# Kernel tuning notes

Measured on AMD Instinct MI355X. Metric: run time of the kernel, lower is better.

Reference implementation:

```python
import jax, jax.numpy as jnp
import numpy as np

B, N, D, H = 16, 4096, 768, 16
E = D // H  # head dim = 48
EPS = 1e-12  # F.normalize eps


def setup_inputs() -> dict:
    key = jax.random.key(0)
    ks = jax.random.split(key, 10)
    s = 0.02
    return {
        "x": jax.random.normal(ks[0], (B, N, D), dtype=jnp.float32),
        "wq": jax.random.normal(ks[1], (D, D), dtype=jnp.float32) * s,
        "bq": jnp.zeros((D,), dtype=jnp.float32),
        "wk": jax.random.normal(ks[2], (D, D), dtype=jnp.float32) * s,
        "bk": jnp.zeros((D,), dtype=jnp.float32),
        "wv": jax.random.normal(ks[3], (D, D), dtype=jnp.float32) * s,
        "bv": jnp.zeros((D,), dtype=jnp.float32),
        "wo": jax.random.normal(ks[4], (D, D), dtype=jnp.float32) * s,
        "bo": jnp.zeros((D,), dtype=jnp.float32),
        "tau": jnp.float32(H),  # scalar learnable temperature, init = num_heads
    }


def _l2norm_seq(t):
    # F.normalize(t, p=2, dim=1): normalize over sequence axis n of [b, n, h, e]
    nrm = jnp.sqrt(jnp.sum(t * t, axis=1, keepdims=True))
    return t / jnp.maximum(nrm, EPS)


def reference(x, wq, bq, wk, bk, wv, bv, wo, bo, tau):
    b, n, d = x.shape
    q = (x @ wq.T + bq).reshape(b, n, H, E)
    k = (x @ wk.T + bk).reshape(b, n, H, E)
    v = (x @ wv.T + bv).reshape(b, n, H, E)
    q = _l2norm_seq(q)
    k = _l2norm_seq(k)
    # cross-covariance attention over feature dim: [b, e, h, q]
    energy = jnp.einsum('bnhe,bnhq->behq', q, k)
    attn = jax.nn.softmax(energy, axis=-1)
    out = jnp.einsum('behq,bnhe->bnhq', attn / tau, v)  # [b, n, h, e]
    out = out.reshape(b, n, d)
    return out @ wo.T + bo
```

## Files before the change

kernel.cpp:

```cpp
#include <hip/hip_runtime.h>
#include <hip/hip_bf16.h>

typedef __attribute__((ext_vector_type(8))) short bf16x8_t;
typedef __attribute__((ext_vector_type(4))) float f32x4_t;
typedef __attribute__((ext_vector_type(4))) float fv4;
typedef __attribute__((ext_vector_type(4))) unsigned short us4_t;
typedef __attribute__((ext_vector_type(8))) unsigned short us8_t;

static constexpr int BB = 16, NN = 4096, DD = 768, HH = 16, EE = 48;

__device__ __forceinline__ unsigned short f2bf(float f) {
  unsigned int u = __float_as_uint(f);
  u += 0x7fffu + ((u >> 16) & 1u);
  return (unsigned short)(u >> 16);
}
__device__ __forceinline__ float bf2f(unsigned short s) {
  unsigned int u = ((unsigned int)s) << 16;
  return __uint_as_float(u);
}

__device__ __forceinline__ void load_lds16(const void* g, void* l) {
  __builtin_amdgcn_global_load_lds((const __attribute__((address_space(1))) void*)g,
                                   (__attribute__((address_space(3))) void*)l, 16, 0, 0);
}

template<int WRITE_THRU>
__device__ __forceinline__ void tcast64(const float* __restrict__ src, int sld,
                                        unsigned short* __restrict__ dst, int dld,
                                        unsigned short* __restrict__ thru, int tld, int t)
{
  __shared__ float L[64][65];
#pragma unroll
  for (int q = 0; q < 4; ++q) {
    const int fi = t + q * 256;
    const int r = fi >> 4, c4 = fi & 15;
    fv4 v = *(const fv4*)(src + (long)r * sld + c4 * 4);
    L[r][c4 * 4 + 0] = v.x; L[r][c4 * 4 + 1] = v.y;
    L[r][c4 * 4 + 2] = v.z; L[r][c4 * 4 + 3] = v.w;
    if (WRITE_THRU) {
      us4_t o; o.x = f2bf(v.x); o.y = f2bf(v.y); o.z = f2bf(v.z); o.w = f2bf(v.w);
      *(us4_t*)(thru + (long)r * tld + c4 * 4) = o;
    }
  }
  __syncthreads();
#pragma unroll
  for (int q = 0; q < 2; ++q) {
    const int wi = t + q * 256;
    const int rr = wi >> 3, ng = wi & 7;
    us8_t o;
#pragma unroll
    for (int j = 0; j < 8; ++j) o[j] = f2bf(L[ng * 8 + j][rr]);
    *(us8_t*)(dst + (long)rr * dld + ng * 8) = o;
  }
  __syncthreads();
}

__global__ __launch_bounds__(256) void transpose_cast_x(
    const float* __restrict__ x, unsigned short* __restrict__ xb,
    unsigned short* __restrict__ xbT)
{
  const int nx = blockIdx.x, dx = blockIdx.y, b = blockIdx.z;
  const int n0 = nx * 64, d0 = dx * 64;
  const float* src = x + ((long)b * NN + n0) * DD + d0;
  unsigned short* thru = xb + ((long)b * NN + n0) * DD + d0;
  unsigned short* dst = xbT + ((long)b * DD + d0) * NN + n0;
  tcast64<1>(src, DD, dst, NN, thru, DD, threadIdx.x);
}

__global__ __launch_bounds__(256) void small_cast(
    const float* __restrict__ wq, const float* __restrict__ wk, const float* __restrict__ wv,
    unsigned short* __restrict__ W2, unsigned short* __restrict__ wvT,
    float* __restrict__ zeros)
{
  const int blk = blockIdx.x, t = threadIdx.x;
  if (blk < 576) {
#pragma unroll
    for (int q = 0; q < 2; ++q) {
      long g = (long)blk * 512 + t * 2 + q;
      long e0 = g * 4;
      int row = (int)(e0 / DD), col = (int)(e0 % DD);
      const float* src = (row < DD) ? (wq + (long)row * DD + col)
                                    : (wk + (long)(row - DD) * DD + col);
      fv4 v = *(const fv4*)src;
      us4_t o; o.x = f2bf(v.x); o.y = f2bf(v.y); o.z = f2bf(v.z); o.w = f2bf(v.w);
      *(us4_t*)(W2 + e0) = o;
    }
  } else if (blk < 720) {
    const int tile = blk - 576;
    const int ti = tile / 12, tj = tile % 12;
    const int k0 = ti * 64, i0 = tj * 64;
    tcast64<0>(wv + (long)i0 * DD + k0, DD, wvT + (long)k0 * DD + i0, DD, nullptr, 0, t);
  } else {
#pragma unroll
    for (int q = 0; q < 4; ++q) zeros[t * 4 + q] = 0.f;
  }
}

__global__ __launch_bounds__(256) void colsum(
    const unsigned short* __restrict__ xbT, float* __restrict__ xsum)
{
  const int bx = blockIdx.x, b = blockIdx.y;
  const int wave = threadIdx.x >> 6, lane = threadIdx.x & 63;
  const int d = bx * 4 + wave;
  const unsigned short* row = xbT + ((long)b * DD + d) * NN;
  float s = 0.f;
#pragma unroll
  for (int it = 0; it < 8; ++it) {
    us8_t v = *(const us8_t*)(row + (it * 64 + lane) * 8);
#pragma unroll
    for (int j = 0; j < 8; ++j) s += bf2f(v[j]);
  }
#pragma unroll
  for (int off = 32; off > 0; off >>= 1) s += __shfl_down(s, off);
  if (lane == 0) xsum[(long)b * DD + d] = s;
}

template<int OUT_BF16>
__global__ __launch_bounds__(256) void gemm_bt(
    const unsigned short* __restrict__ A, int lda, long aStride,
    const unsigned short* __restrict__ Bt, int ldb, long bStride,
    void* __restrict__ Cv, int ldc, long cStride,
    const float* __restrict__ bias, long biasStride, int K)
{
  __shared__ unsigned short As[128 * 32];
  __shared__ unsigned short Bs[128 * 32];
  const int zb = blockIdx.z;
  const unsigned short* Ab = A + (long)zb * aStride;
  const unsigned short* Bb = Bt + (long)zb * bStride;
  const float* bz = bias + (long)zb * biasStride;
  const long m0 = (long)blockIdx.x * 128;
  const int n0 = blockIdx.y * 128;
  const int t = threadIdx.x;
  const int wave = t >> 6, lane = t & 63;
  const int wr = wave >> 1, wc = wave & 1;

  f32x4_t acc[4][4] = {};

  const int o0 = t * 16;
  const int row0 = o0 >> 6, kc0 = (o0 & 63) >> 1;
  const int o1 = 4096 + t * 16;
  const int row1 = o1 >> 6, kc1 = (o1 & 63) >> 1;
  unsigned short* ldsA = As + wave * 512;
  unsigned short* ldsB = Bs + wave * 512;

  for (int kt = 0; kt < K; kt += 32) {
    load_lds16(Ab + (m0 + row0) * (long)lda + kt + kc0, ldsA);
    load_lds16(Ab + (m0 + row1) * (long)lda + kt + kc1, ldsA + 2048);
    load_lds16(Bb + (long)(n0 + row0) * ldb + kt + kc0, ldsB);
    load_lds16(Bb + (long)(n0 + row1) * ldb + kt + kc1, ldsB + 2048);
    __syncthreads();
    bf16x8_t af[4], bfr[4];
    const int kofs = (lane >> 4) << 3;
#pragma unroll
    for (int f = 0; f < 4; ++f) {
      af[f]  = *(const bf16x8_t*)&As[(wr * 64 + f * 16 + (lane & 15)) * 32 + kofs];
      bfr[f] = *(const bf16x8_t*)&Bs[(wc * 64 + f * 16 + (lane & 15)) * 32 + kofs];
    }
#pragma unroll
    for (int i = 0; i < 4; ++i)
#pragma unroll
      for (int j = 0; j < 4; ++j)
        acc[i][j] = __builtin_amdgcn_mfma_f32_16x16x32_bf16(af[i], bfr[j], acc[i][j], 0, 0, 0);
    __syncthreads();
  }

  const int col_l = lane & 15;
  const int rbase = (lane >> 4) << 2;
#pragma unroll
  for (int i = 0; i < 4; ++i) {
#pragma unroll
    for (int r = 0; r < 4; ++r) {
      const long grow = m0 + wr * 64 + i * 16 + rbase + r;
      if (OUT_BF16) {
        unsigned short* crow = (unsigned short*)Cv + (long)zb * cStride + grow * ldc + n0 + wc * 64;
#pragma unroll
        for (int j = 0; j < 4; ++j) {
          int col = j * 16 + col_l;
          crow[col] = f2bf(acc[i][j][r] + bz[n0 + wc * 64 + col]);
        }
      } else {
        float* crow = (float*)Cv + (long)zb * cStride + grow * ldc + n0 + wc * 64;
#pragma unroll
        for (int j = 0; j < 4; ++j) {
          int col = j * 16 + col_l;
          crow[col] = acc[i][j][r] + bz[n0 + wc * 64 + col];
        }
      }
    }
  }
}

#define GP_STRIDE 2464

__global__ __launch_bounds__(256) void energy_partial2(
    const unsigned short* __restrict__ T, const unsigned short* __restrict__ W2,
    float* __restrict__ Gp)
{
  __shared__ unsigned short Ts[2][48 * 128];
  __shared__ unsigned short Ws[2][48 * 128];
  __shared__ float G_sh[2448];

  const int kc = blockIdx.x, h = blockIdx.y, b = blockIdx.z;
  const int t = threadIdx.x;
  const int wave = t >> 6, lane = t & 63;

  for (int i = t; i < 2448; i += 256) G_sh[i] = 0.f;

  f32x4_t accG[3][3] = {};
  f32x4_t accQ[3] = {};
  f32x4_t accK[3] = {};

  long qoff[3];
#pragma unroll
  for (int p = 0; p < 3; ++p) {
    const int L = p * 4096 + wave * 1024 + lane * 16;
    const int e = L >> 8;
    const int blk = (L >> 4) & 15;
    const int sblk = blk ^ (e & 7);
    qoff[p] = (long)e * DD + sblk * 8;
  }
  const unsigned short* Tq = T + ((long)b * 1536 + h * 48) * DD;
  const unsigned short* Tk = Tq + (long)DD * DD;
  const unsigned short* Wq = W2 + (long)h * 48 * DD;
  const unsigned short* Wk = Wq + (long)DD * DD;

  int foff[3];
#pragma unroll
  for (int f = 0; f < 3; ++f) {
    const int e = f * 16 + (lane & 15);
    foff[f] = e * 256 + (((wave * 4 + (lane >> 4)) ^ (e & 7)) << 4);
  }
  __syncthreads();

  for (int ci = 0; ci < 3; ++ci) {
    const int col0 = kc * 384 + ci * 128;
#pragma unroll
    for (int p = 0; p < 3; ++p) {
      load_lds16(Tq + qoff[p] + col0, &Ts[0][p * 2048] + wave * 512);
      load_lds16(Tk + qoff[p] + col0, &Ts[1][p * 2048] + wave * 512);
      load_lds16(Wq + qoff[p] + col0, &Ws[0][p * 2048] + wave * 512);
      load_lds16(Wk + qoff[p] + col0, &Ws[1][p * 2048] + wave * 512);
    }
    __syncthreads();
    bf16x8_t tq[3], tk[3], wqf[3], wkf[3];
#pragma unroll
    for (int f = 0; f < 3; ++f) {
      tq[f]  = *(const bf16x8_t*)((const char*)&Ts[0][0] + foff[f]);
      tk[f]  = *(const bf16x8_t*)((const char*)&Ts[1][0] + foff[f]);
      wqf[f] = *(const bf16x8_t*)((const char*)&Ws[0][0] + foff[f]);
      wkf[f] = *(const bf16x8_t*)((const char*)&Ws[1][0] + foff[f]);
    }
#pragma unroll
    for (int i = 0; i < 3; ++i) {
      accQ[i] = __builtin_amdgcn_mfma_f32_16x16x32_bf16(tq[i], wqf[i], accQ[i], 0, 0, 0);
      accK[i] = __builtin_amdgcn_mfma_f32_16x16x32_bf16(tk[i], wkf[i], accK[i], 0, 0, 0);
#pragma unroll
      for (int j = 0; j < 3; ++j)
        accG[i][j] = __builtin_amdgcn_mfma_f32_16x16x32_bf16(tq[i], wkf[j], accG[i][j], 0, 0, 0);
    }
    __syncthreads();
  }

#pragma unroll
  for (int i = 0; i < 3; ++i)
#pragma unroll
    for (int j = 0; j < 3; ++j) {
      int e = i * 16 + ((lane >> 4) << 2);
      int qi = j * 16 + (lane & 15);
#pragma unroll
      for (int r = 0; r < 4; ++r) atomicAdd(&G_sh[(e + r) * 49 + qi], accG[i][j][r]);
    }
  if ((lane >> 4) == ((lane & 15) >> 2)) {
    int r = (lane & 15) & 3;
#pragma unroll
    for (int f = 0; f < 3; ++f) {
      atomicAdd(&G_sh[2352 + f * 16 + (lane & 15)], accQ[f][r]);
      atomicAdd(&G_sh[2400 + f * 16 + (lane & 15)], accK[f][r]);
    }
  }
  __syncthreads();

  float* out = Gp + (long)(((b * HH + h) << 1) + kc) * GP_STRIDE;
  for (int i = t; i < 2448; i += 256) out[i] = G_sh[i];
}

__global__ __launch_bounds__(256) void energy_finish2(
    const float* __restrict__ Gp, const float* __restrict__ xsum,
    const float* __restrict__ wq, const float* __restrict__ wk,
    const float* __restrict__ bq, const float* __restrict__ bk,
    const float* __restrict__ tau_p, unsigned short* __restrict__ A_out)
{
  __shared__ float G_sh[2448];
  __shared__ float vq[48], vk[48], bqs[48], bks[48];
  __shared__ int has_bias;
  const int h = blockIdx.x, b = blockIdx.y;
  const int t = threadIdx.x;

  const float* base = Gp + (long)((b * HH + h) << 1) * GP_STRIDE;
  for (int i = t; i < 2448; i += 256)
    G_sh[i] = base[i] + base[GP_STRIDE + i];
  if (t < 48) { bqs[t] = bq[h * 48 + t]; bks[t] = bk[h * 48 + t]; }
  __syncthreads();
  if (t == 0) {
    float s = 0.f;
    for (int i = 0; i < 48; ++i) s += fabsf(bqs[i]) + fabsf(bks[i]);
    has_bias = (s != 0.f);
  }
  __syncthreads();
  if (has_bias) {
    if (t < 96) {
      const int e = t < 48 ? t : t - 48;
      const float* wrow = (t < 48 ? wq : wk) + (long)(h * 48 + e) * DD;
      const float* xs = xsum + (long)b * DD;
      float s = 0.f;
      for (int g = 0; g < DD / 4; ++g) {
        fv4 a = *(const fv4*)(wrow + g * 4);
        fv4 c = *(const fv4*)(xs + g * 4);
        s += a.x * c.x + a.y * c.y + a.z * c.z + a.w * c.w;
      }
      if (t < 48) vq[e] = s; else vk[e] = s;
    }
  } else if (t < 48) { vq[t] = 0.f; vk[t] = 0.f; }
  __syncthreads();

  if (t < 48) {
    const float tau = *tau_p;
    const float nq2c = G_sh[2352 + t] + 2.f * bqs[t] * vq[t] + (float)NN * bqs[t] * bqs[t];
    const float nq = fmaxf(sqrtf(nq2c), 1e-12f);
    float row[48];
    float mx = -1e30f;
#pragma unroll 1
    for (int qi = 0; qi < 48; ++qi) {
      float nk2c = G_sh[2400 + qi] + 2.f * bks[qi] * vk[qi] + (float)NN * bks[qi] * bks[qi];
      float nk = fmaxf(sqrtf(nk2c), 1e-12f);
      float e = G_sh[t * 49 + qi] + vq[t] * bks[qi] + bqs[t] * vk[qi]
              + (float)NN * bqs[t] * bks[qi];
      float g = e / (nq * nk);
      row[qi] = g; mx = fmaxf(mx, g);
    }
    float s = 0.f;
#pragma unroll 1
    for (int qi = 0; qi < 48; ++qi) { row[qi] = __expf(row[qi] - mx); s += row[qi]; }
    const float inv = 1.f / (s * tau);
    unsigned short* dst = A_out + (((long)b * HH + h) * 48) * 64 + (long)t * 64;
#pragma unroll 1
    for (int qi = 0; qi < 48; ++qi) dst[qi] = f2bf(row[qi] * inv);
#pragma unroll 1
    for (int qi = 48; qi < 64; ++qi) dst[qi] = 0;
  }
}

__global__ __launch_bounds__(256) void build_btf(
    const unsigned short* __restrict__ A_ws, const float* __restrict__ wo,
    unsigned short* __restrict__ btf)
{
  __shared__ unsigned short Wsh[128 * 72];
  __shared__ unsigned short Ash[48 * 72];
  const int nchunk = blockIdx.x, h = blockIdx.y, b = blockIdx.z;
  const int t = threadIdx.x;
  const int wave = t >> 6, lane = t & 63;
  const int no0 = nchunk * 128;

  for (int i = t; i < 128 * 64; i += 256) {
    int r = i >> 6, c = i & 63;
    Wsh[r * 72 + c] = (c < 48) ? f2bf(wo[(long)(no0 + r) * DD + h * 48 + c]) : (unsigned short)0;
  }
  const unsigned short* Asrc = A_ws + ((long)b * HH + h) * 48 * 64;
  for (int i = t; i < 48 * 64; i += 256) {
    int r = i >> 6, c = i & 63;
    Ash[r * 72 + c] = Asrc[r * 64 + c];
  }
  __syncthreads();

  f32x4_t acc[2][3] = {};
#pragma unroll
  for (int ks = 0; ks < 2; ++ks) {
    const int k0 = ks * 32 + ((lane >> 4) << 3);
    bf16x8_t af[2], bfr[3];
#pragma unroll
    for (int mi = 0; mi < 2; ++mi)
      af[mi] = *(const bf16x8_t*)&Wsh[(wave * 32 + mi * 16 + (lane & 15)) * 72 + k0];
#pragma unroll
    for (int nj = 0; nj < 3; ++nj)
      bfr[nj] = *(const bf16x8_t*)&Ash[(nj * 16 + (lane & 15)) * 72 + k0];
#pragma unroll
    for (int mi = 0; mi < 2; ++mi)
#pragma unroll
      for (int nj = 0; nj < 3; ++nj)
        acc[mi][nj] = __builtin_amdgcn_mfma_f32_16x16x32_bf16(af[mi], bfr[nj], acc[mi][nj], 0, 0, 0);
  }

  const int col_l = lane & 15;
  const int rbase = (lane >> 4) << 2;
#pragma unroll
  for (int mi = 0; mi < 2; ++mi)
#pragma unroll
    for (int r = 0; r < 4; ++r) {
      int no = no0 + wave * 32 + mi * 16 + rbase + r;
      unsigned short* dst = btf + ((long)b * DD + no) * DD + h * 48;
#pragma unroll
      for (int nj = 0; nj < 3; ++nj)
        dst[nj * 16 + col_l] = f2bf(acc[mi][nj][r]);
    }
}

__global__ __launch_bounds__(256) void build_bias2(
    const unsigned short* __restrict__ btf, const float* __restrict__ bv,
    const float* __restrict__ bo, float* __restrict__ bias2)
{
  const int bx = blockIdx.x, b = blockIdx.y;
  const int wave = threadIdx.x >> 6, lane = threadIdx.x & 63;
  const int j = bx * 4 + wave;
  const unsigned short* row = btf + ((long)b * DD + j) * DD;
  float s = 0.f;
#pragma unroll
  for (int ii = 0; ii < 12; ++ii) {
    int i = ii * 64 + lane;
    s += bf2f(row[i]) * bv[i];
  }
#pragma unroll
  for (int off = 32; off > 0; off >>= 1) s += __shfl_down(s, off);
  if (lane == 0) bias2[(long)b * DD + j] = bo[j] + s;
}

extern "C" void kernel_launch(void* const* d_in, const int* in_sizes, int n_in,
                              void* d_out, int out_size, void* d_ws, size_t ws_size,
                              hipStream_t stream)
{
  (void)in_sizes; (void)n_in; (void)out_size;
  const float* x   = (const float*)d_in[0];
  const float* wq  = (const float*)d_in[1];
  const float* bq  = (const float*)d_in[2];
  const float* wk  = (const float*)d_in[3];
  const float* bk  = (const float*)d_in[4];
  const float* wv  = (const float*)d_in[5];
  const float* bv  = (const float*)d_in[6];
  const float* wo  = (const float*)d_in[7];
  const float* bo  = (const float*)d_in[8];
  const float* tau = (const float*)d_in[9];

  char* ws = (char*)d_ws;
  unsigned short* xb    = (unsigned short*)(ws + 0L);
  unsigned short* xbT   = (unsigned short*)(ws + 100663296L);
  unsigned short* S     = (unsigned short*)(ws + 201326592L);
  unsigned short* T     = (unsigned short*)(ws + 220200960L);
  unsigned short* W2    = (unsigned short*)(ws + 257949696L);
  unsigned short* wvT   = (unsigned short*)(ws + 260308992L);
  float*          zeros = (float*)         (ws + 261488640L);
  float*          xsum  = (float*)         (ws + 261492736L);
  float*          Gp    = (float*)         (ws + 261541888L);
  unsigned short* A_ws  = (unsigned short*)(ws + 266588160L);
  unsigned short* btf   = (unsigned short*)(ws + 268161024L);
  unsigned short* Ctf   = (unsigned short*)(ws + 287035392L);
  float*          bias2 = (float*)         (ws + 305909760L);
  if (ws_size < 305958912ULL) return;

  transpose_cast_x<<<dim3(64, 12, BB), 256, 0, stream>>>(x, xb, xbT);
  small_cast<<<721, 256, 0, stream>>>(wq, wk, wv, W2, wvT, zeros);
  colsum<<<dim3(192, BB), 256, 0, stream>>>(xbT, xsum);

  gemm_bt<1><<<dim3(6, 6, BB), 256, 0, stream>>>(
      xbT, NN, (long)DD * NN, xbT, NN, (long)DD * NN,
      S, DD, (long)DD * DD, zeros, 0L, NN);

  gemm_bt<1><<<dim3(12, 6, BB), 256, 0, stream>>>(
      W2, DD, 0L, S, DD, (long)DD * DD,
      T, DD, (long)1536 * DD, zeros, 0L, DD);

  energy_partial2<<<dim3(2, HH, BB), 256, 0, stream>>>(T, W2, Gp);
  energy_finish2<<<dim3(HH, BB), 256, 0, stream>>>(Gp, xsum, wq, wk, bq, bk, tau, A_ws);

  build_btf<<<dim3(6, HH, BB), 256, 0, stream>>>(A_ws, wo, btf);
  build_bias2<<<dim3(192, BB), 256, 0, stream>>>(btf, bv, bo, bias2);

  gemm_bt<1><<<dim3(6, 6, BB), 256, 0, stream>>>(
      btf, DD, (long)DD * DD, wvT, DD, 0L,
      Ctf, DD, (long)DD * DD, zeros, 0L, DD);

  gemm_bt<0><<<dim3(32, 6, BB), 256, 0, stream>>>(
      xb, DD, (long)NN * DD, Ctf, DD, (long)DD * DD,
      d_out, DD, (long)NN * DD, bias2, (long)DD, DD);
}
```

Before: 561.7 us.

## Exploit Gram matrix symmetry and remap GEMM blocks for XCD locality

Flattens every GEMM launch to a 1D grid and remaps block ids so that consecutive work items go to the same XCD (bid&7 striding), which should improve L2 reuse within each batch. For the x^T x Gram GEMM it computes only the upper-triangular 128x128 tiles (21 of 36) and writes each off-diagonal tile twice, once transposed, cutting that GEMM's MFMA work. The epilogue is reordered so bias is loaded once per column, and the mirrored store is written as 4-element vectors. The risks are the transposed stores being less coalesced and the grid sizes now needing to be divisible by 8 for the remap to be a valid permutation.

Measured after the change: 509.7 us. -9.3%, faster.

```diff
diff --git a/kernel.cpp b/kernel.cpp
--- a/kernel.cpp
+++ b/kernel.cpp
@@ -115,21 +115,34 @@
   if (lane == 0) xsum[(long)b * DD + d] = s;
 }
 
-template<int OUT_BF16>
+template<int OUT_BF16, int SYM>
 __global__ __launch_bounds__(256) void gemm_bt(
     const unsigned short* __restrict__ A, int lda, long aStride,
     const unsigned short* __restrict__ Bt, int ldb, long bStride,
     void* __restrict__ Cv, int ldc, long cStride,
-    const float* __restrict__ bias, long biasStride, int K)
+    const float* __restrict__ bias, long biasStride, int K,
+    int perB, int nt)
 {
   __shared__ unsigned short As[128 * 32];
   __shared__ unsigned short Bs[128 * 32];
-  const int zb = blockIdx.z;
+  const int nwg = gridDim.x;
+  const int bid = blockIdx.x;
+  const int wid = (bid & 7) * (nwg >> 3) + (bid >> 3);
+  const int zb = wid / perB;
+  const int t0 = wid % perB;
+  int i0, j0;
+  if (SYM) {
+    int tt = t0; i0 = 0;
+    while (tt >= nt - i0) { tt -= nt - i0; ++i0; }
+    j0 = i0 + tt;
+  } else {
+    i0 = t0 / nt; j0 = t0 % nt;
+  }
   const unsigned short* Ab = A + (long)zb * aStride;
   const unsigned short* Bb = Bt + (long)zb * bStride;
   const float* bz = bias + (long)zb * biasStride;
-  const long m0 = (long)blockIdx.x * 128;
-  const int n0 = blockIdx.y * 128;
+  const long m0 = (long)i0 * 128;
+  const int n0 = j0 * 128;
   const int t = threadIdx.x;
   const int wave = t >> 6, lane = t & 63;
   const int wr = wave >> 1, wc = wave & 1;
@@ -168,22 +181,25 @@
   const int rbase = (lane >> 4) << 2;
 #pragma unroll
   for (int i = 0; i < 4; ++i) {
-#pragma unroll
-    for (int r = 0; r < 4; ++r) {
-      const long grow = m0 + wr * 64 + i * 16 + rbase + r;
+    const long growb = m0 + wr * 64 + i * 16 + rbase;
+#pragma unroll
+    for (int j = 0; j < 4; ++j) {
+      const int col = n0 + wc * 64 + j * 16 + col_l;
       if (OUT_BF16) {
-        unsigned short* crow = (unsigned short*)Cv + (long)zb * cStride + grow * ldc + n0 + wc * 64;
-#pragma unroll
-        for (int j = 0; j < 4; ++j) {
-          int col = j * 16 + col_l;
-          crow[col] = f2bf(acc[i][j][r] + bz[n0 + wc * 64 + col]);
-        }
+        const float bcol = bz[col];
+        us4_t o;
+#pragma unroll
+        for (int r = 0; r < 4; ++r) o[r] = f2bf(acc[i][j][r] + bcol);
+        unsigned short* cb = (unsigned short*)Cv + (long)zb * cStride;
+#pragma unroll
+        for (int r = 0; r < 4; ++r) cb[(growb + r) * ldc + col] = o[r];
+        if (SYM && i0 != j0)
+          *(us4_t*)(cb + (long)col * ldc + growb) = o;
       } else {
-        float* crow = (float*)Cv + (long)zb * cStride + grow * ldc + n0 + wc * 64;
-#pragma unroll
-        for (int j = 0; j < 4; ++j) {
-          int col = j * 16 + col_l;
-          crow[col] = acc[i][j][r] + bz[n0 + wc * 64 + col];
+#pragma unroll
+        for (int r = 0; r < 4; ++r) {
+          float* crow = (float*)Cv + (long)zb * cStride + (growb + r) * ldc;
+          crow[col] = acc[i][j][r] + bz[col];
         }
       }
     }
@@ -459,13 +475,13 @@
   small_cast<<<721, 256, 0, stream>>>(wq, wk, wv, W2, wvT, zeros);
   colsum<<<dim3(192, BB), 256, 0, stream>>>(xbT, xsum);
 
-  gemm_bt<1><<<dim3(6, 6, BB), 256, 0, stream>>>(
+  gemm_bt<1, 1><<<16 * 21, 256, 0, stream>>>(
       xbT, NN, (long)DD * NN, xbT, NN, (long)DD * NN,
-      S, DD, (long)DD * DD, zeros, 0L, NN);
-
-  gemm_bt<1><<<dim3(12, 6, BB), 256, 0, stream>>>(
+      S, DD, (long)DD * DD, zeros, 0L, NN, 21, 6);
+
+  gemm_bt<1, 0><<<16 * 72, 256, 0, stream>>>(
       W2, DD, 0L, S, DD, (long)DD * DD,
-      T, DD, (long)1536 * DD, zeros, 0L, DD);
+      T, DD, (long)1536 * DD, zeros, 0L, DD, 72, 6);
 
   energy_partial2<<<dim3(2, HH, BB), 256, 0, stream>>>(T, W2, Gp);
   energy_finish2<<<dim3(HH, BB), 256, 0, stream>>>(Gp, xsum, wq, wk, bq, bk, tau, A_ws);
@@ -473,11 +489,11 @@
   build_btf<<<dim3(6, HH, BB), 256, 0, stream>>>(A_ws, wo, btf);
   build_bias2<<<dim3(192, BB), 256, 0, stream>>>(btf, bv, bo, bias2);
 
-  gemm_bt<1><<<dim3(6, 6, BB), 256, 0, stream>>>(
+  gemm_bt<1, 0><<<16 * 36, 256, 0, stream>>>(
       btf, DD, (long)DD * DD, wvT, DD, 0L,
-      Ctf, DD, (long)DD * DD, zeros, 0L, DD);
-
-  gemm_bt<0><<<dim3(32, 6, BB), 256, 0, stream>>>(
+      Ctf, DD, (long)DD * DD, zeros, 0L, DD, 36, 6);
+
+  gemm_bt<0, 0><<<16 * 192, 256, 0, stream>>>(
       xb, DD, (long)NN * DD, Ctf, DD, (long)DD * DD,
-      d_out, DD, (long)NN * DD, bias2, (long)DD, DD);
-}
+      d_out, DD, (long)NN * DD, bias2, (long)DD, DD, 192, 6);
+}
```
